# Kernel tuning notes

Measured on AMD Instinct MI355X. Metric: run time of the kernel, lower is better.

Reference implementation:

```python
import jax, jax.numpy as jnp
import numpy as np

N = 50000       # nodes
E = 1200000     # edges (before self-loops)
IN_CH = 128
HID = 64
L = 3           # FAConv layers
EPS_RES = 0.1   # FAConv eps residual weight
BN_EPS = 1e-5


def _bn(x, g, b):
    # BatchNorm1d, training-mode statistics (biased variance, like torch)
    mu = x.mean(axis=0)
    var = x.var(axis=0)
    return g * (x - mu) * jax.lax.rsqrt(var + BN_EPS) + b


def setup_inputs() -> dict:
    key = jax.random.key(0)
    ks = jax.random.split(key, 12)
    s = lambda d: 1.0 / np.sqrt(d)
    H2 = HID // 2
    return {
        "x": jax.random.normal(ks[0], (N, IN_CH), jnp.float32),
        "edge_index": jax.random.randint(ks[1], (2, E), 0, N, dtype=jnp.int32),
        "batch_size": 10000,
        "W_in": jax.random.normal(ks[2], (IN_CH, HID), jnp.float32) * s(IN_CH),
        "b_in": jnp.zeros((HID,), jnp.float32),
        "att_l": jax.random.normal(ks[3], (L, HID), jnp.float32) * s(HID),
        "att_r": jax.random.normal(ks[4], (L, HID), jnp.float32) * s(HID),
        "bn_g": jnp.ones((L, HID), jnp.float32),
        "bn_b": jnp.zeros((L, HID), jnp.float32),
        "W1": jax.random.normal(ks[5], (HID, HID), jnp.float32) * s(HID),
        "b1": jnp.zeros((HID,), jnp.float32),
        "g1": jnp.ones((HID,), jnp.float32),
        "be1": jnp.zeros((HID,), jnp.float32),
        "W2": jax.random.normal(ks[6], (HID, H2), jnp.float32) * s(HID),
        "b2": jnp.zeros((H2,), jnp.float32),
        "g2": jnp.ones((H2,), jnp.float32),
        "be2": jnp.zeros((H2,), jnp.float32),
        "W3": jax.random.normal(ks[7], (H2, 1), jnp.float32) * s(H2),
        "b3": jnp.zeros((1,), jnp.float32),
    }


def reference(x, edge_index, batch_size, W_in, b_in, att_l, att_r, bn_g, bn_b,
              W1, b1, g1, be1, W2, b2, g2, be2, W3, b3):
    n = x.shape[0]
    # gcn_norm with self-loops (same for all layers since graph is fixed)
    loops = jnp.arange(n, dtype=edge_index.dtype)
    src = jnp.concatenate([edge_index[0], loops])  # j (source)
    dst = jnp.concatenate([edge_index[1], loops])  # i (target)
    deg = jax.ops.segment_sum(jnp.ones_like(dst, dtype=x.dtype), dst, num_segments=n)
    dinv = jnp.where(deg > 0, jax.lax.rsqrt(deg), 0.0)
    norm = dinv[src] * dinv[dst]                   # [E+N]

    x0 = jax.nn.relu(x @ W_in + b_in)              # [N, HID]
    h = x0
    for l in range(L):
        al = h @ att_l[l]                          # [N] att_l^T x
        ar = h @ att_r[l]                          # [N] att_r^T x
        alpha = jnp.tanh(al[src] + ar[dst])        # [E+N] signed attention
        msg = h[src] * (alpha * norm)[:, None]     # gather + weight
        out = jax.ops.segment_sum(msg, dst, num_segments=n) + EPS_RES * x0
        h = _bn(jax.nn.relu(out), bn_g[l], bn_b[l])

    z = h[:batch_size]
    z = jax.nn.relu(_bn(z @ W1 + b1, g1, be1))
    z = jax.nn.relu(_bn(z @ W2 + b2, g2, be2))
    return (z @ W3 + b3).squeeze(-1)
```

## Files before the change

kernel.cpp:

```cpp
#include <hip/hip_runtime.h>
#include <hip/hip_bf16.h>
#include <math.h>

#define NND 50000
#define NE  1200000
#define TOT (NE + NND)
#define INCH 128
#define HID 64
#define H2  32
#define NL  3
#define BSZ 10000
#define NB  196
#define NHB 128
#define NSTAT 256
#define CHUNK 4096
#define EPS_RES 0.1f
#define BN_EPS 1e-5f

typedef unsigned short ushort8v __attribute__((ext_vector_type(8)));

__device__ __forceinline__ float b2f(unsigned short u) {
    return __uint_as_float((unsigned)u << 16);
}


__global__ __launch_bounds__(256) void bhist_kernel(const int* __restrict__ dst, int* __restrict__ bh_part, int ne) {
    __shared__ int arr[256];
    arr[threadIdx.x] = 0;
    __syncthreads();
    int i = blockIdx.x * 256 + threadIdx.x;
    int stride = gridDim.x * 256;
    for (int e = i; e < ne; e += stride) atomicAdd(&arr[dst[e] >> 8], 1);
    __syncthreads();
    bh_part[blockIdx.x * 256 + threadIdx.x] = arr[threadIdx.x];
}

__global__ __launch_bounds__(256) void bscan_kernel(const int* __restrict__ bh_part,
                                                    int* __restrict__ bstart, int* __restrict__ bcur,
                                                    int* __restrict__ offsets) {
    __shared__ int ls[256];
    int t = threadIdx.x;
    int v = 0;
    for (int k = 0; k < NHB; k++) v += bh_part[k * 256 + t];
    ls[t] = v;
    __syncthreads();
    for (int off = 1; off < 256; off <<= 1) {
        int tv = (t >= off) ? ls[t - off] : 0;
        __syncthreads();
        ls[t] += tv;
        __syncthreads();
    }
    int excl = ls[t] - v;
    if (t < NB) { bstart[t] = excl; bcur[t] = excl; }
    if (t == NB) bstart[NB] = ls[NB - 1];
    if (t == 0) offsets[NND] = TOT;
}

__global__ __launch_bounds__(256) void passA_kernel(const int* __restrict__ src, const int* __restrict__ dst,
                                                    int* __restrict__ bcur, unsigned* __restrict__ ebuf, int ne) {
    __shared__ int arr[256];
    int t = threadIdx.x;
    int base = blockIdx.x * CHUNK;
    int lim = min(base + CHUNK, ne);
    arr[t] = 0;
    __syncthreads();
    for (int e = base + t; e < lim; e += 256) atomicAdd(&arr[dst[e] >> 8], 1);
    __syncthreads();
    int cnt_t = arr[t];
    int claimed = 0;
    if (cnt_t > 0) claimed = atomicAdd(&bcur[t], cnt_t);
    __syncthreads();
    arr[t] = claimed;
    __syncthreads();
    for (int e = base + t; e < lim; e += 256) {
        int d = dst[e];
        int pos = atomicAdd(&arr[d >> 8], 1);
        ebuf[pos] = ((unsigned)src[e] << 8) | (unsigned)(d & 255);
    }
}

__global__ __launch_bounds__(256) void bucket_build_kernel(const unsigned* __restrict__ ebuf, const int* __restrict__ bstart,
                                                           int* __restrict__ offsets, int* __restrict__ csr,
                                                           float* __restrict__ dinv) {
    __shared__ int dcnt[256];
    __shared__ int ls[256];
    __shared__ int cur[256];
    int b = blockIdx.x, t = threadIdx.x;
    dcnt[t] = 0;
    __syncthreads();
    int beg = bstart[b], end = bstart[b + 1];
    for (int p = beg + t; p < end; p += 256) atomicAdd(&dcnt[ebuf[p] & 255u], 1);
    __syncthreads();
    int node = b * 256 + t;
    bool valid = node < NND;
    int d = valid ? (dcnt[t] + 1) : 0;
    ls[t] = d;
    __syncthreads();
    for (int off = 1; off < 256; off <<= 1) {
        int tv = (t >= off) ? ls[t - off] : 0;
        __syncthreads();
        ls[t] += tv;
        __syncthreads();
    }
    int off = bstart[b] + b * 256 + ls[t] - d;
    if (valid) {
        offsets[node] = off;
        dinv[node] = rsqrtf((float)d);
        csr[off] = node;
        cur[t] = off + 1;
    }
    __syncthreads();
    for (int p = beg + t; p < end; p += 256) {
        unsigned ed = ebuf[p];
        int pos = atomicAdd(&cur[ed & 255u], 1);
        csr[pos] = (int)(ed >> 8);
    }
}

__global__ __launch_bounds__(256) void gemm_in_kernel(const float* __restrict__ x, const float* __restrict__ W,
                                                      const float* __restrict__ b,
                                                      const float* __restrict__ attl, const float* __restrict__ attr,
                                                      __hip_bfloat16* __restrict__ x0bf,
                                                      float* __restrict__ al, float* __restrict__ ar) {
    __shared__ float Wl[INCH * HID];
    __shared__ float xs[16 * INCH];
    int t = threadIdx.x;
    for (int i = t; i < INCH * HID; i += 256) Wl[i] = W[i];
    size_t rowbase = (size_t)blockIdx.x * 16;
    for (int i = t; i < 16 * INCH; i += 256) xs[i] = x[rowbase * INCH + i];
    __syncthreads();
    int col = t & 63, rg = t >> 6;
    float a0 = 0.f, a1 = 0.f, a2 = 0.f, a3 = 0.f;
    for (int k = 0; k < INCH; k++) {
        float wk = Wl[k * HID + col];
        a0 = fmaf(xs[(rg * 4 + 0) * INCH + k], wk, a0);
        a1 = fmaf(xs[(rg * 4 + 1) * INCH + k], wk, a1);
        a2 = fmaf(xs[(rg * 4 + 2) * INCH + k], wk, a2);
        a3 = fmaf(xs[(rg * 4 + 3) * INCH + k], wk, a3);
    }
    float bb = b[col];
    a0 = fmaxf(a0 + bb, 0.f); a1 = fmaxf(a1 + bb, 0.f);
    a2 = fmaxf(a2 + bb, 0.f); a3 = fmaxf(a3 + bb, 0.f);
    size_t r = rowbase + rg * 4;
    x0bf[(r + 0) * HID + col] = __float2bfloat16(a0);
    x0bf[(r + 1) * HID + col] = __float2bfloat16(a1);
    x0bf[(r + 2) * HID + col] = __float2bfloat16(a2);
    x0bf[(r + 3) * HID + col] = __float2bfloat16(a3);
    float wl = attl[col], wr = attr[col];
    float p0 = a0 * wl, q0 = a0 * wr, p1 = a1 * wl, q1 = a1 * wr;
    float p2 = a2 * wl, q2 = a2 * wr, p3 = a3 * wl, q3 = a3 * wr;
    for (int off = 32; off > 0; off >>= 1) {
        p0 += __shfl_xor(p0, off); q0 += __shfl_xor(q0, off);
        p1 += __shfl_xor(p1, off); q1 += __shfl_xor(q1, off);
        p2 += __shfl_xor(p2, off); q2 += __shfl_xor(q2, off);
        p3 += __shfl_xor(p3, off); q3 += __shfl_xor(q3, off);
    }
    if (col == 0) {
        al[r + 0] = p0; ar[r + 0] = q0;
        al[r + 1] = p1; ar[r + 1] = q1;
        al[r + 2] = p2; ar[r + 2] = q2;
        al[r + 3] = p3; ar[r + 3] = q3;
    }
}

__global__ __launch_bounds__(256) void aggregate_kernel(const __hip_bfloat16* __restrict__ hbf,
                                                        const __hip_bfloat16* __restrict__ x0bf,
                                                        const float* __restrict__ al, const float* __restrict__ ar,
                                                        const float* __restrict__ dinv,
                                                        const int* __restrict__ offsets, const int* __restrict__ csr,
                                                        float* __restrict__ y, int n) {
    int v = (blockIdx.x * 256 + threadIdx.x) >> 6;
    int lane = threadIdx.x & 63;
    if (v >= n) return;
    int g = lane >> 3;
    int cl = (lane & 7) << 3;
    int beg = offsets[v], end = offsets[v + 1];
    float arv = ar[v];
    float a0 = 0.f, a1 = 0.f, a2 = 0.f, a3 = 0.f, a4 = 0.f, a5 = 0.f, a6 = 0.f, a7 = 0.f;
    for (int base = beg; base < end; base += 64) {
        int p = base + lane;
        int u = 0; float c = 0.f;
        if (p < end) {
            u = csr[p];
            c = tanhf(al[u] + arv) * dinv[u];
        }
        int cnt = min(64, end - base);
        int iters = (cnt + 7) >> 3;
        for (int it = 0; it < iters; ++it) {
            int j = (it << 3) + g;
            int js = (j < cnt) ? j : 0;
            int uj = __shfl(u, js);
            float cj = __shfl(c, js);
            if (j < cnt) {
                ushort8v hv = *(const ushort8v*)((const unsigned short*)hbf + (size_t)uj * HID + cl);
                a0 = fmaf(b2f(hv[0]), cj, a0);
                a1 = fmaf(b2f(hv[1]), cj, a1);
                a2 = fmaf(b2f(hv[2]), cj, a2);
                a3 = fmaf(b2f(hv[3]), cj, a3);
                a4 = fmaf(b2f(hv[4]), cj, a4);
                a5 = fmaf(b2f(hv[5]), cj, a5);
                a6 = fmaf(b2f(hv[6]), cj, a6);
                a7 = fmaf(b2f(hv[7]), cj, a7);
            }
        }
    }
    for (int off = 8; off < 64; off <<= 1) {
        a0 += __shfl_xor(a0, off); a1 += __shfl_xor(a1, off);
        a2 += __shfl_xor(a2, off); a3 += __shfl_xor(a3, off);
        a4 += __shfl_xor(a4, off); a5 += __shfl_xor(a5, off);
        a6 += __shfl_xor(a6, off); a7 += __shfl_xor(a7, off);
    }
    if (g == 0) {
        float dv = dinv[v];
        ushort8v xb = *(const ushort8v*)((const unsigned short*)x0bf + (size_t)v * HID + cl);
        float4 o0, o1;
        o0.x = fmaxf(fmaf(EPS_RES, b2f(xb[0]), a0 * dv), 0.f);
        o0.y = fmaxf(fmaf(EPS_RES, b2f(xb[1]), a1 * dv), 0.f);
        o0.z = fmaxf(fmaf(EPS_RES, b2f(xb[2]), a2 * dv), 0.f);
        o0.w = fmaxf(fmaf(EPS_RES, b2f(xb[3]), a3 * dv), 0.f);
        o1.x = fmaxf(fmaf(EPS_RES, b2f(xb[4]), a4 * dv), 0.f);
        o1.y = fmaxf(fmaf(EPS_RES, b2f(xb[5]), a5 * dv), 0.f);
        o1.z = fmaxf(fmaf(EPS_RES, b2f(xb[6]), a6 * dv), 0.f);
        o1.w = fmaxf(fmaf(EPS_RES, b2f(xb[7]), a7 * dv), 0.f);
        *(float4*)(y + (size_t)v * HID + cl) = o0;
        *(float4*)(y + (size_t)v * HID + cl + 4) = o1;
    }
}

template <int C>
__global__ __launch_bounds__(256) void bn_stats_fused_kernel(const float* __restrict__ y, int rows,
                                                             const float* __restrict__ g, const float* __restrict__ b,
                                                             float rows_inv,
                                                             float* __restrict__ acc, int* __restrict__ counter,
                                                             float* __restrict__ scale, float* __restrict__ shift) {
    const int TPR = C / 4;
    const int RPW = 64 / TPR;
    int lane = threadIdx.x & 63;
    int wave = threadIdx.x >> 6;
    int cl = (lane % TPR) * 4;
    int rsub = lane / TPR;
    int rpb = 4 * RPW;
    int r = blockIdx.x * rpb + wave * RPW + rsub;
    int stride = gridDim.x * rpb;
    float s0 = 0.f, s1 = 0.f, s2 = 0.f, s3 = 0.f, q0 = 0.f, q1 = 0.f, q2 = 0.f, q3 = 0.f;
    for (; r < rows; r += stride) {
        float4 v = *(const float4*)(y + (size_t)r * C + cl);
        s0 += v.x; q0 = fmaf(v.x, v.x, q0);
        s1 += v.y; q1 = fmaf(v.y, v.y, q1);
        s2 += v.z; q2 = fmaf(v.z, v.z, q2);
        s3 += v.w; q3 = fmaf(v.w, v.w, q3);
    }
    for (int off = TPR; off < 64; off <<= 1) {
        s0 += __shfl_xor(s0, off); q0 += __shfl_xor(q0, off);
        s1 += __shfl_xor(s1, off); q1 += __shfl_xor(q1, off);
        s2 += __shfl_xor(s2, off); q2 += __shfl_xor(q2, off);
        s3 += __shfl_xor(s3, off); q3 += __shfl_xor(q3, off);
    }
    __shared__ float lsum[4][64], lsq[4][64];
    if (lane < TPR) {
        lsum[wave][cl + 0] = s0; lsq[wave][cl + 0] = q0;
        lsum[wave][cl + 1] = s1; lsq[wave][cl + 1] = q1;
        lsum[wave][cl + 2] = s2; lsq[wave][cl + 2] = q2;
        lsum[wave][cl + 3] = s3; lsq[wave][cl + 3] = q3;
    }
    __syncthreads();
    int t = threadIdx.x;
    if (t < C) {
        float ts = lsum[0][t] + lsum[1][t] + lsum[2][t] + lsum[3][t];
        float tq = lsq[0][t] + lsq[1][t] + lsq[2][t] + lsq[3][t];
        atomicAdd(&acc[t], ts);
        atomicAdd(&acc[64 + t], tq);
    }
    __shared__ int islast;
    __syncthreads();
    if (t == 0) {
        __threadfence();
        int old = atomicAdd(counter, 1);
        islast = (old == (int)gridDim.x - 1) ? 1 : 0;
    }
    __syncthreads();
    if (islast && t < C) {
        float ts = atomicAdd(&acc[t], 0.f);
        float tq = atomicAdd(&acc[64 + t], 0.f);
        float mean = ts * rows_inv;
        float var = tq * rows_inv - mean * mean;
        float sc = g[t] * rsqrtf(var + BN_EPS);
        scale[t] = sc;
        shift[t] = b[t] - mean * sc;
        atomicExch(&acc[t], 0.f);
        atomicExch(&acc[64 + t], 0.f);
        if (t == 0) atomicExch(counter, 0);
    }
}

__global__ __launch_bounds__(256) void bnapply_attn_kernel(const float* __restrict__ y, const float* __restrict__ scale,
                                                           const float* __restrict__ shift,
                                                           const float* __restrict__ attl, const float* __restrict__ attr,
                                                           __hip_bfloat16* __restrict__ hbf,
                                                           float* __restrict__ al, float* __restrict__ ar, int n) {
    int v = (blockIdx.x * 256 + threadIdx.x) >> 6;
    int lane = threadIdx.x & 63;
    if (v >= n) return;
    float val = fmaf(y[(size_t)v * HID + lane], scale[lane], shift[lane]);
    hbf[(size_t)v * HID + lane] = __float2bfloat16(val);
    float pl = val * attl[lane];
    float pr = val * attr[lane];
    for (int off = 32; off > 0; off >>= 1) {
        pl += __shfl_xor(pl, off);
        pr += __shfl_xor(pr, off);
    }
    if (lane == 0) { al[v] = pl; ar[v] = pr; }
}

__global__ __launch_bounds__(256) void mlp1_kernel(const float* __restrict__ y, const float* __restrict__ scale,
                                                   const float* __restrict__ shift, const float* __restrict__ W,
                                                   const float* __restrict__ b, float* __restrict__ z1) {
    __shared__ float Wl[HID * HID];
    __shared__ float xs[16 * HID];
    int t = threadIdx.x;
    for (int i = t; i < HID * HID; i += 256) Wl[i] = W[i];
    size_t rowbase = (size_t)blockIdx.x * 16;
    for (int i = t; i < 16 * HID; i += 256) {
        int c = i & 63;
        xs[i] = fmaf(y[rowbase * HID + i], scale[c], shift[c]);
    }
    __syncthreads();
    int col = t & 63, rg = t >> 6;
    float a0 = 0.f, a1 = 0.f, a2 = 0.f, a3 = 0.f;
    for (int k = 0; k < HID; k++) {
        float wk = Wl[k * HID + col];
        a0 = fmaf(xs[(rg * 4 + 0) * HID + k], wk, a0);
        a1 = fmaf(xs[(rg * 4 + 1) * HID + k], wk, a1);
        a2 = fmaf(xs[(rg * 4 + 2) * HID + k], wk, a2);
        a3 = fmaf(xs[(rg * 4 + 3) * HID + k], wk, a3);
    }
    float bb = b[col];
    size_t r = rowbase + rg * 4;
    z1[(r + 0) * HID + col] = a0 + bb;
    z1[(r + 1) * HID + col] = a1 + bb;
    z1[(r + 2) * HID + col] = a2 + bb;
    z1[(r + 3) * HID + col] = a3 + bb;
}

__global__ __launch_bounds__(256) void mlp2_kernel(const float* __restrict__ z1, const float* __restrict__ scale,
                                                   const float* __restrict__ shift, const float* __restrict__ W,
                                                   const float* __restrict__ b, float* __restrict__ z2) {
    __shared__ float Wl[HID * H2];
    __shared__ float as[16 * HID];
    int t = threadIdx.x;
    for (int i = t; i < HID * H2; i += 256) Wl[i] = W[i];
    size_t rowbase = (size_t)blockIdx.x * 16;
    for (int i = t; i < 16 * HID; i += 256) {
        int c = i & 63;
        float v = z1[rowbase * HID + i];
        as[i] = fmaxf(fmaf(v, scale[c], shift[c]), 0.f);
    }
    __syncthreads();
    int col = t & 31, rg = t >> 5;
    float a0 = 0.f, a1 = 0.f;
    for (int k = 0; k < HID; k++) {
        float wk = Wl[k * H2 + col];
        a0 = fmaf(as[(rg * 2 + 0) * HID + k], wk, a0);
        a1 = fmaf(as[(rg * 2 + 1) * HID + k], wk, a1);
    }
    float bb = b[col];
    size_t r = rowbase + rg * 2;
    z2[(r + 0) * H2 + col] = a0 + bb;
    z2[(r + 1) * H2 + col] = a1 + bb;
}

__global__ __launch_bounds__(256) void mlp3_kernel(const float* __restrict__ z2, const float* __restrict__ scale,
                                                   const float* __restrict__ shift, const float* __restrict__ W3,
                                                   const float* __restrict__ b3, float* __restrict__ out, int rows) {
    int i = blockIdx.x * 256 + threadIdx.x;
    if (i >= rows) return;
    float acc = 0.f;
#pragma unroll
    for (int k = 0; k < H2; k++) {
        float v = fmaxf(fmaf(z2[(size_t)i * H2 + k], scale[k], shift[k]), 0.f);
        acc = fmaf(v, W3[k], acc);
    }
    out[i] = acc + b3[0];
}

extern "C" void kernel_launch(void* const* d_in, const int* in_sizes, int n_in,
                              void* d_out, int out_size, void* d_ws, size_t ws_size,
                              hipStream_t stream) {
    const float* x     = (const float*)d_in[0];
    const int*   ei    = (const int*)d_in[1];
    const int*   src   = ei;
    const int*   dst   = ei + NE;
    const float* W_in  = (const float*)d_in[3];
    const float* b_in  = (const float*)d_in[4];
    const float* att_l = (const float*)d_in[5];
    const float* att_r = (const float*)d_in[6];
    const float* bn_g  = (const float*)d_in[7];
    const float* bn_b  = (const float*)d_in[8];
    const float* W1    = (const float*)d_in[9];
    const float* b1    = (const float*)d_in[10];
    const float* g1    = (const float*)d_in[11];
    const float* be1   = (const float*)d_in[12];
    const float* W2    = (const float*)d_in[13];
    const float* b2    = (const float*)d_in[14];
    const float* g2    = (const float*)d_in[15];
    const float* be2   = (const float*)d_in[16];
    const float* W3    = (const float*)d_in[17];
    const float* b3    = (const float*)d_in[18];
    float* out = (float*)d_out;

    char* p = (char*)d_ws;
    auto carve = [&](size_t bytes) -> void* {
        void* r = (void*)p;
        p += (bytes + 255) & ~(size_t)255;
        return r;
    };
    int*   bh_part = (int*)carve((size_t)NHB * 256 * 4);
    int*   bstart  = (int*)carve(256 * 4);
    int*   bcur    = (int*)carve(256 * 4);
    int*   offsets = (int*)carve((size_t)(NND + 1) * 4);
    int*   csr     = (int*)carve((size_t)TOT * 4);
    float* dinv    = (float*)carve((size_t)NND * 4);
    float* al      = (float*)carve((size_t)NND * 4);
    float* ar      = (float*)carve((size_t)NND * 4);
    __hip_bfloat16* x0bf = (__hip_bfloat16*)carve((size_t)NND * HID * 2);
    __hip_bfloat16* hbfA = (__hip_bfloat16*)carve((size_t)NND * HID * 2);
    __hip_bfloat16* hbfB = (__hip_bfloat16*)carve((size_t)NND * HID * 2);
    float* ybuf    = (float*)carve((size_t)NND * HID * 4);
    unsigned* ebuf = (unsigned*)ybuf;
    float* acc     = (float*)carve(132 * 4);
    int*   counter = (int*)(acc + 128);
    float* scale   = (float*)carve(64 * 4);
    float* shift   = (float*)carve(64 * 4);
    float* z1      = (float*)carve((size_t)BSZ * HID * 4);
    float* z2      = (float*)carve((size_t)BSZ * H2 * 4);

    const int nblkA = (NE + CHUNK - 1) / CHUNK;

    hipMemsetAsync(acc, 0, 132 * 4, stream);

    bhist_kernel<<<NHB, 256, 0, stream>>>(dst, bh_part, NE);
    gemm_in_kernel<<<NND / 16, 256, 0, stream>>>(x, W_in, b_in, att_l, att_r, x0bf, al, ar);
    bscan_kernel<<<1, 256, 0, stream>>>(bh_part, bstart, bcur, offsets);
    passA_kernel<<<nblkA, 256, 0, stream>>>(src, dst, bcur, ebuf, NE);
    bucket_build_kernel<<<NB, 256, 0, stream>>>(ebuf, bstart, offsets, csr, dinv);

    const __hip_bfloat16* h_in = x0bf;
    __hip_bfloat16* hbufs[2] = {hbfA, hbfB};
    for (int l = 0; l < NL; l++) {
        aggregate_kernel<<<NND / 4, 256, 0, stream>>>(h_in, x0bf, al, ar, dinv, offsets, csr, ybuf, NND);
        bn_stats_fused_kernel<64><<<NSTAT, 256, 0, stream>>>(ybuf, NND, bn_g + l * HID, bn_b + l * HID,
                                                             1.0f / NND, acc, counter, scale, shift);
        if (l < NL - 1) {
            bnapply_attn_kernel<<<NND / 4, 256, 0, stream>>>(ybuf, scale, shift,
                                                             att_l + (l + 1) * HID, att_r + (l + 1) * HID,
                                                             hbufs[l], al, ar, NND);
            h_in = hbufs[l];
        }
    }

    mlp1_kernel<<<BSZ / 16, 256, 0, stream>>>(ybuf, scale, shift, W1, b1, z1);
    bn_stats_fused_kernel<64><<<NSTAT, 256, 0, stream>>>(z1, BSZ, g1, be1, 1.0f / BSZ, acc, counter, scale, shift);

    mlp2_kernel<<<BSZ / 16, 256, 0, stream>>>(z1, scale, shift, W2, b2, z2);
    bn_stats_fused_kernel<32><<<NSTAT, 256, 0, stream>>>(z2, BSZ, g2, be2, 1.0f / BSZ, acc, counter, scale, shift);

    mlp3_kernel<<<(BSZ + 255) / 256, 256, 0, stream>>>(z2, scale, shift, W3, b3, out, BSZ);
}
```

Measured before the change: 385.1 us.

## Precompute per-edge attention coefficients into packed buffer and simplify aggregation

Adds a per-edge coefficient kernel that computes tanh(al[u]+ar[v])*dinv[u] once per layer and stores it alongside the source index as an int2. The aggregation kernel then reads these pairs directly, dropping the shuffle broadcast and tanh work. Each row is now split across 16 lanes of 4 channels instead of 8 lanes of 8. A destination map is emitted during CSR build, and tanh is replaced by a clamped exp-based approximation. The cost is an extra pass over all edges per layer and more global memory traffic for the vmap and uc buffers, plus narrower 8-byte gathers.

```diff
diff --git a/kernel.cpp b/kernel.cpp
--- a/kernel.cpp
+++ b/kernel.cpp
@@ -18,9 +18,16 @@
 #define BN_EPS 1e-5f
 
 typedef unsigned short ushort8v __attribute__((ext_vector_type(8)));
+typedef unsigned short ushort4v __attribute__((ext_vector_type(4)));
 
 __device__ __forceinline__ float b2f(unsigned short u) {
     return __uint_as_float((unsigned)u << 16);
+}
+
+__device__ __forceinline__ float fast_tanh(float x) {
+    float cx = fminf(fmaxf(x, -8.f), 8.f);
+    float e = __expf(2.f * cx);
+    return 1.f - __fdividef(2.f, e + 1.f);
 }
 
 
@@ -81,6 +88,7 @@
 
 __global__ __launch_bounds__(256) void bucket_build_kernel(const unsigned* __restrict__ ebuf, const int* __restrict__ bstart,
                                                            int* __restrict__ offsets, int* __restrict__ csr,
+                                                           int* __restrict__ vmap,
                                                            float* __restrict__ dinv) {
     __shared__ int dcnt[256];
     __shared__ int ls[256];
@@ -107,6 +115,7 @@
         offsets[node] = off;
         dinv[node] = rsqrtf((float)d);
         csr[off] = node;
+        vmap[off] = node;
         cur[t] = off + 1;
     }
     __syncthreads();
@@ -114,7 +123,19 @@
         unsigned ed = ebuf[p];
         int pos = atomicAdd(&cur[ed & 255u], 1);
         csr[pos] = (int)(ed >> 8);
-    }
+        vmap[pos] = b * 256 + (int)(ed & 255u);
+    }
+}
+
+__global__ __launch_bounds__(256) void coeff_kernel(const int* __restrict__ csr, const int* __restrict__ vmap,
+                                                    const float* __restrict__ al, const float* __restrict__ ar,
+                                                    const float* __restrict__ dinv, int2* __restrict__ uc, int tot) {
+    int p = blockIdx.x * 256 + threadIdx.x;
+    if (p >= tot) return;
+    int u = csr[p];
+    int v = vmap[p];
+    float c = fast_tanh(al[u] + ar[v]) * dinv[u];
+    uc[p] = make_int2(u, __float_as_int(c));
 }
 
 __global__ __launch_bounds__(256) void gemm_in_kernel(const float* __restrict__ x, const float* __restrict__ W,
@@ -165,65 +186,45 @@
 
 __global__ __launch_bounds__(256) void aggregate_kernel(const __hip_bfloat16* __restrict__ hbf,
                                                         const __hip_bfloat16* __restrict__ x0bf,
-                                                        const float* __restrict__ al, const float* __restrict__ ar,
+                                                        const int2* __restrict__ uc,
                                                         const float* __restrict__ dinv,
-                                                        const int* __restrict__ offsets, const int* __restrict__ csr,
+                                                        const int* __restrict__ offsets,
                                                         float* __restrict__ y, int n) {
     int v = (blockIdx.x * 256 + threadIdx.x) >> 6;
     int lane = threadIdx.x & 63;
     if (v >= n) return;
-    int g = lane >> 3;
-    int cl = (lane & 7) << 3;
+    int g = lane >> 4;
+    int cl = (lane & 15) << 2;
     int beg = offsets[v], end = offsets[v + 1];
-    float arv = ar[v];
-    float a0 = 0.f, a1 = 0.f, a2 = 0.f, a3 = 0.f, a4 = 0.f, a5 = 0.f, a6 = 0.f, a7 = 0.f;
-    for (int base = beg; base < end; base += 64) {
-        int p = base + lane;
-        int u = 0; float c = 0.f;
-        if (p < end) {
-            u = csr[p];
-            c = tanhf(al[u] + arv) * dinv[u];
+    int cnt = end - beg;
+    float a0 = 0.f, a1 = 0.f, a2 = 0.f, a3 = 0.f;
+    int iters = (cnt + 3) >> 2;
+    for (int it = 0; it < iters; ++it) {
+        int j = (it << 2) + g;
+        if (j < cnt) {
+            int2 pe = uc[beg + j];
+            float cj = __int_as_float(pe.y);
+            const unsigned short* hp = (const unsigned short*)hbf + (size_t)pe.x * HID + cl;
+            ushort4v hv = *(const ushort4v*)hp;
+            a0 = fmaf(b2f(hv[0]), cj, a0);
+            a1 = fmaf(b2f(hv[1]), cj, a1);
+            a2 = fmaf(b2f(hv[2]), cj, a2);
+            a3 = fmaf(b2f(hv[3]), cj, a3);
         }
-        int cnt = min(64, end - base);
-        int iters = (cnt + 7) >> 3;
-        for (int it = 0; it < iters; ++it) {
-            int j = (it << 3) + g;
-            int js = (j < cnt) ? j : 0;
-            int uj = __shfl(u, js);
-            float cj = __shfl(c, js);
-            if (j < cnt) {
-                ushort8v hv = *(const ushort8v*)((const unsigned short*)hbf + (size_t)uj * HID + cl);
-                a0 = fmaf(b2f(hv[0]), cj, a0);
-                a1 = fmaf(b2f(hv[1]), cj, a1);
-                a2 = fmaf(b2f(hv[2]), cj, a2);
-                a3 = fmaf(b2f(hv[3]), cj, a3);
-                a4 = fmaf(b2f(hv[4]), cj, a4);
-                a5 = fmaf(b2f(hv[5]), cj, a5);
-                a6 = fmaf(b2f(hv[6]), cj, a6);
-                a7 = fmaf(b2f(hv[7]), cj, a7);
-            }
-        }
-    }
-    for (int off = 8; off < 64; off <<= 1) {
+    }
+    for (int off = 16; off < 64; off <<= 1) {
         a0 += __shfl_xor(a0, off); a1 += __shfl_xor(a1, off);
         a2 += __shfl_xor(a2, off); a3 += __shfl_xor(a3, off);
-        a4 += __shfl_xor(a4, off); a5 += __shfl_xor(a5, off);
-        a6 += __shfl_xor(a6, off); a7 += __shfl_xor(a7, off);
     }
     if (g == 0) {
         float dv = dinv[v];
-        ushort8v xb = *(const ushort8v*)((const unsigned short*)x0bf + (size_t)v * HID + cl);
-        float4 o0, o1;
-        o0.x = fmaxf(fmaf(EPS_RES, b2f(xb[0]), a0 * dv), 0.f);
-        o0.y = fmaxf(fmaf(EPS_RES, b2f(xb[1]), a1 * dv), 0.f);
-        o0.z = fmaxf(fmaf(EPS_RES, b2f(xb[2]), a2 * dv), 0.f);
-        o0.w = fmaxf(fmaf(EPS_RES, b2f(xb[3]), a3 * dv), 0.f);
-        o1.x = fmaxf(fmaf(EPS_RES, b2f(xb[4]), a4 * dv), 0.f);
-        o1.y = fmaxf(fmaf(EPS_RES, b2f(xb[5]), a5 * dv), 0.f);
-        o1.z = fmaxf(fmaf(EPS_RES, b2f(xb[6]), a6 * dv), 0.f);
-        o1.w = fmaxf(fmaf(EPS_RES, b2f(xb[7]), a7 * dv), 0.f);
-        *(float4*)(y + (size_t)v * HID + cl) = o0;
-        *(float4*)(y + (size_t)v * HID + cl + 4) = o1;
+        ushort4v xb = *(const ushort4v*)((const unsigned short*)x0bf + (size_t)v * HID + cl);
+        float4 o;
+        o.x = fmaxf(fmaf(EPS_RES, b2f(xb[0]), a0 * dv), 0.f);
+        o.y = fmaxf(fmaf(EPS_RES, b2f(xb[1]), a1 * dv), 0.f);
+        o.z = fmaxf(fmaf(EPS_RES, b2f(xb[2]), a2 * dv), 0.f);
+        o.w = fmaxf(fmaf(EPS_RES, b2f(xb[3]), a3 * dv), 0.f);
+        *(float4*)(y + (size_t)v * HID + cl) = o;
     }
 }
 
@@ -419,6 +420,8 @@
     int*   bcur    = (int*)carve(256 * 4);
     int*   offsets = (int*)carve((size_t)(NND + 1) * 4);
     int*   csr     = (int*)carve((size_t)TOT * 4);
+    int*   vmap    = (int*)carve((size_t)TOT * 4);
+    int2*  uc      = (int2*)carve((size_t)TOT * 8);
     float* dinv    = (float*)carve((size_t)NND * 4);
     float* al      = (float*)carve((size_t)NND * 4);
     float* ar      = (float*)carve((size_t)NND * 4);
@@ -435,6 +438,7 @@
     float* z2      = (float*)carve((size_t)BSZ * H2 * 4);
 
     const int nblkA = (NE + CHUNK - 1) / CHUNK;
+    const int nblkC = (TOT + 255) / 256;
 
     hipMemsetAsync(acc, 0, 132 * 4, stream);
 
@@ -442,18 +446,21 @@
     gemm_in_kernel<<<NND / 16, 256, 0, stream>>>(x, W_in, b_in, att_l, att_r, x0bf, al, ar);
     bscan_kernel<<<1, 256, 0, stream>>>(bh_part, bstart, bcur, offsets);
     passA_kernel<<<nblkA, 256, 0, stream>>>(src, dst, bcur, ebuf, NE);
-    bucket_build_kernel<<<NB, 256, 0, stream>>>(ebuf, bstart, offsets, csr, dinv);
+    bucket_build_kernel<<<NB, 256, 0, stream>>>(ebuf, bstart, offsets, csr, vmap, dinv);
+
+    coeff_kernel<<<nblkC, 256, 0, stream>>>(csr, vmap, al, ar, dinv, uc, TOT);
 
     const __hip_bfloat16* h_in = x0bf;
     __hip_bfloat16* hbufs[2] = {hbfA, hbfB};
     for (int l = 0; l < NL; l++) {
-        aggregate_kernel<<<NND / 4, 256, 0, stream>>>(h_in, x0bf, al, ar, dinv, offsets, csr, ybuf, NND);
+        aggregate_kernel<<<NND / 4, 256, 0, stream>>>(h_in, x0bf, uc, dinv, offsets, ybuf, NND);
         bn_stats_fused_kernel<64><<<NSTAT, 256, 0, stream>>>(ybuf, NND, bn_g + l * HID, bn_b + l * HID,
                                                              1.0f / NND, acc, counter, scale, shift);
         if (l < NL - 1) {
             bnapply_attn_kernel<<<NND / 4, 256, 0, stream>>>(ybuf, scale, shift,
                                                              att_l + (l + 1) * HID, att_r + (l + 1) * HID,
                                                              hbufs[l], al, ar, NND);
+            coeff_kernel<<<nblkC, 256, 0, stream>>>(csr, vmap, al, ar, dinv, uc, TOT);
             h_in = hbufs[l];
         }
     }
```

Result: slower. 455.0 us (+18.2%).
